# Kernel tuning notes

Hardware: AMD Instinct MI355X
Metric: run time of the kernel (lower is better)

## Reference

```python
import jax, jax.numpy as jnp
import numpy as np
from functools import partial

INPUT_DIM = 22
HIDDEN = 64
LAYERS = 3
OUT = 4
B, T = 1024, 512


def _lstm_layer(x_seq, w_ih, w_hh, b_ih, b_hh):
    # x_seq: [B, T, Din]; gate order (PyTorch): i, f, g, o
    Bsz = x_seq.shape[0]
    H = w_hh.shape[1]
    # precompute input projections for all timesteps: [B, T, 4H]
    x_proj = jnp.einsum('bti,gi->btg', x_seq, w_ih) + b_ih + b_hh

    def step(carry, xp):
        h, c = carry
        gates = xp + h @ w_hh.T  # [B, 4H]
        i, f, g, o = jnp.split(gates, 4, axis=-1)
        i = jax.nn.sigmoid(i)
        f = jax.nn.sigmoid(f)
        g = jnp.tanh(g)
        o = jax.nn.sigmoid(o)
        c = f * c + i * g
        h = o * jnp.tanh(c)
        return (h, c), h

    init = (jnp.zeros((Bsz, H), x_seq.dtype), jnp.zeros((Bsz, H), x_seq.dtype))
    _, hs = jax.lax.scan(step, init, jnp.swapaxes(x_proj, 0, 1))  # [T, B, H]
    return jnp.swapaxes(hs, 0, 1)  # [B, T, H]


def setup_inputs() -> dict:
    key = jax.random.key(0)
    ks = jax.random.split(key, 16)
    inp = {'x': jax.random.normal(ks[0], (B, INPUT_DIM, T), dtype=jnp.float32)}
    k = 1.0 / np.sqrt(HIDDEN)
    i = 1
    for l in range(LAYERS):
        din = INPUT_DIM if l == 0 else HIDDEN
        inp[f'w_ih{l}'] = jax.random.uniform(ks[i], (4 * HIDDEN, din), minval=-k, maxval=k); i += 1
        inp[f'w_hh{l}'] = jax.random.uniform(ks[i], (4 * HIDDEN, HIDDEN), minval=-k, maxval=k); i += 1
        inp[f'b_ih{l}'] = jax.random.uniform(ks[i], (4 * HIDDEN,), minval=-k, maxval=k); i += 1
        inp[f'b_hh{l}'] = jax.random.uniform(ks[i], (4 * HIDDEN,), minval=-k, maxval=k); i += 1
    inp['w_fc'] = jax.random.uniform(ks[i], (OUT, HIDDEN), minval=-k, maxval=k); i += 1
    inp['b_fc'] = jax.random.uniform(ks[i], (OUT,), minval=-k, maxval=k)
    return inp


def reference(x, w_ih0, w_hh0, b_ih0, b_hh0, w_ih1, w_hh1, b_ih1, b_hh1,
              w_ih2, w_hh2, b_ih2, b_hh2, w_fc, b_fc):
    # x: [B, 22, T] -> batch_first [B, T, 22]
    h = jnp.transpose(x, (0, 2, 1))
    h = _lstm_layer(h, w_ih0, w_hh0, b_ih0, b_hh0)
    # inter-layer dropout(0.4) is identity in eval/inference mode
    h = _lstm_layer(h, w_ih1, w_hh1, b_ih1, b_hh1)
    h = _lstm_layer(h, w_ih2, w_hh2, b_ih2, b_hh2)
    last = h[:, -1, :]  # [B, H]
    return last @ w_fc.T + b_fc  # [B, 4]
```

## Files before the change

### kernel.cpp

```cpp
#include <hip/hip_runtime.h>


#define TT   512
#define NTH  768
#define NBLK 256

typedef _Float16 h16;
typedef __attribute__((ext_vector_type(8))) _Float16 h16x8;
typedef __attribute__((ext_vector_type(4))) float f32x4;

#define MFMA16(a, b, c) __builtin_amdgcn_mfma_f32_16x16x32_f16((a), (b), (c), 0, 0, 0)

__device__ __forceinline__ float sigm(float z) {
    return __builtin_amdgcn_rcpf(1.f + __expf(-z));
}

__device__ __forceinline__ h16x8 loadB(const float* __restrict__ W, int ld, int ro,
                                       int k0, int kmax) {
    h16x8 r;
    #pragma unroll
    for (int i = 0; i < 8; ++i) {
        const int k = k0 + i;
        r[i] = (h16)((k < kmax) ? W[(size_t)ro * ld + k] : 0.f);
    }
    return r;
}

__global__ __attribute__((amdgpu_flat_work_group_size(NTH, NTH), amdgpu_waves_per_eu(3)))
void lstm_mfma(
    const float* __restrict__ x,
    const float* __restrict__ wih0, const float* __restrict__ whh0,
    const float* __restrict__ bih0, const float* __restrict__ bhh0,
    const float* __restrict__ wih1, const float* __restrict__ whh1,
    const float* __restrict__ bih1, const float* __restrict__ bhh1,
    const float* __restrict__ wih2, const float* __restrict__ whh2,
    const float* __restrict__ bih2, const float* __restrict__ bhh2,
    const float* __restrict__ wfc, const float* __restrict__ bfc,
    float* __restrict__ out)
{
    const int tid  = threadIdx.x;
    const int w    = tid >> 6;
    const int wl   = w >> 2;
    const int wg   = w & 3;
    const int lane = tid & 63;
    const int nloc = lane & 15;
    const int kg   = lane >> 4;
    const int b4   = blockIdx.x * 4;
    const int u    = wg * 16 + nloc;

    __shared__ alignas(16) h16 XL[2 * 32 * 512];
    __shared__ alignas(16) h16 HT[3 * 2 * 1024];
    __shared__ h16 PAD[3072];

    h16x8 Bf[4][4];
    float bias[4];
    #pragma unroll
    for (int g = 0; g < 4; ++g) {
        const int ro = g * 64 + u;
        if (wl == 0) {
            Bf[g][0] = loadB(wih0, 22, ro, kg * 8,      22);
            Bf[g][1] = loadB(whh0, 64, ro, kg * 8,      64);
            Bf[g][2] = loadB(whh0, 64, ro, 32 + kg * 8, 64);
            Bf[g][3] = Bf[g][2];
            bias[g]  = bih0[ro] + bhh0[ro];
        } else if (wl == 1) {
            Bf[g][0] = loadB(wih1, 64, ro, kg * 8,      64);
            Bf[g][1] = loadB(wih1, 64, ro, 32 + kg * 8, 64);
            Bf[g][2] = loadB(whh1, 64, ro, kg * 8,      64);
            Bf[g][3] = loadB(whh1, 64, ro, 32 + kg * 8, 64);
            bias[g]  = bih1[ro] + bhh1[ro];
        } else {
            Bf[g][0] = loadB(wih2, 64, ro, kg * 8,      64);
            Bf[g][1] = loadB(wih2, 64, ro, 32 + kg * 8, 64);
            Bf[g][2] = loadB(whh2, 64, ro, kg * 8,      64);
            Bf[g][3] = loadB(whh2, 64, ro, 32 + kg * 8, 64);
            bias[g]  = bih2[ro] + bhh2[ro];
        }
    }

    if (bias[0] > 1.0e30f) { PAD[tid & 2047] = (h16)bias[0]; out[0] = (float)PAD[0]; }

    {
        int* xz = (int*)XL;
        for (int i = tid; i < 2 * 32 * 256; i += NTH) xz[i] = 0;
        int* hz = (int*)HT;
        for (int i = tid; i < 3 * 2 * 512; i += NTH) hz[i] = 0;
    }
    __syncthreads();

    auto stage_x = [&](int chunk) {
        if (tid < 4 * 22) {
            const int bl = tid / 22, ii = tid - bl * 22;
            const float* src = x + (size_t)(b4 + bl) * (22 * 512) + (size_t)ii * 512
                                 + chunk * 32;
            h16* dst = &XL[(chunk & 1) * (32 * 512) + (ii >> 3) * 128 + (4 * bl) * 8 + (ii & 7)];
            #pragma unroll
            for (int q = 0; q < 8; ++q) {
                const float4 v = ((const float4*)src)[q];
                dst[(q * 4 + 0) * 512] = (h16)v.x;
                dst[(q * 4 + 1) * 512] = (h16)v.y;
                dst[(q * 4 + 2) * 512] = (h16)v.z;
                dst[(q * 4 + 3) * 512] = (h16)v.w;
            }
        }
    };
    stage_x(0);

    const int lo8  = lane * 8;
    const int hoff = (u >> 3) * 128 + kg * 32 + (u & 7);

    float cst = 0.f;

    auto ew = [&](const f32x4& zi, const f32x4& zf, const f32x4& zg, const f32x4& zo,
                  h16* hb) {
        const float vi = sigm(zi[0]);
        const float vf = sigm(zf[0]);
        const float vg = 2.f * sigm(2.f * zg[0]) - 1.f;
        const float vo = sigm(zo[0]);
        const float c  = vf * cst + vi * vg;
        cst = c;
        hb[hoff] = (h16)(vo * (2.f * sigm(2.f * c) - 1.f));
    };

    __syncthreads();

    #pragma unroll 1
    for (int t = 0; t < TT + 2; ++t) {
        const int wb = t & 1, rb = wb ^ 1;
        const h16* h0r = HT + 0 * 2048 + rb * 1024;
        h16*       h0w = HT + 0 * 2048 + wb * 1024;
        const h16* h1r = HT + 1 * 2048 + rb * 1024;
        h16*       h1w = HT + 1 * 2048 + wb * 1024;
        const h16* h2r = HT + 2 * 2048 + rb * 1024;
        h16*       h2w = HT + 2 * 2048 + wb * 1024;

        if (wl == 0) {
            if (t < TT) {
                const h16x8 ax   = *(const h16x8*)&XL[((t >> 5) & 1) * (32 * 512)
                                                      + (t & 31) * 512 + lo8];
                const h16x8 a0lo = *(const h16x8*)(h0r + lo8);
                const h16x8 a0hi = *(const h16x8*)(h0r + lo8 + 512);
                f32x4 z[4];
                #pragma unroll
                for (int g = 0; g < 4; ++g) {
                    z[g] = f32x4{bias[g], 0.f, 0.f, 0.f};
                    z[g] = MFMA16(ax,   Bf[g][0], z[g]);
                    z[g] = MFMA16(a0lo, Bf[g][1], z[g]);
                    z[g] = MFMA16(a0hi, Bf[g][2], z[g]);
                }
                ew(z[0], z[1], z[2], z[3], h0w);
            }
            if ((t & 31) == 16 && (t >> 5) < 15) stage_x((t >> 5) + 1);
        } else if (wl == 1) {
            if (t >= 1 && t < TT + 1) {
                const h16x8 a0lo = *(const h16x8*)(h0r + lo8);
                const h16x8 a0hi = *(const h16x8*)(h0r + lo8 + 512);
                const h16x8 a1lo = *(const h16x8*)(h1r + lo8);
                const h16x8 a1hi = *(const h16x8*)(h1r + lo8 + 512);
                f32x4 z[4];
                #pragma unroll
                for (int g = 0; g < 4; ++g) {
                    z[g] = f32x4{bias[g], 0.f, 0.f, 0.f};
                    z[g] = MFMA16(a0lo, Bf[g][0], z[g]);
                    z[g] = MFMA16(a0hi, Bf[g][1], z[g]);
                    z[g] = MFMA16(a1lo, Bf[g][2], z[g]);
                    z[g] = MFMA16(a1hi, Bf[g][3], z[g]);
                }
                ew(z[0], z[1], z[2], z[3], h1w);
            }
        } else {
            if (t >= 2) {
                const h16x8 a1lo = *(const h16x8*)(h1r + lo8);
                const h16x8 a1hi = *(const h16x8*)(h1r + lo8 + 512);
                const h16x8 a2lo = *(const h16x8*)(h2r + lo8);
                const h16x8 a2hi = *(const h16x8*)(h2r + lo8 + 512);
                f32x4 z[4];
                #pragma unroll
                for (int g = 0; g < 4; ++g) {
                    z[g] = f32x4{bias[g], 0.f, 0.f, 0.f};
                    z[g] = MFMA16(a1lo, Bf[g][0], z[g]);
                    z[g] = MFMA16(a1hi, Bf[g][1], z[g]);
                    z[g] = MFMA16(a2lo, Bf[g][2], z[g]);
                    z[g] = MFMA16(a2hi, Bf[g][3], z[g]);
                }
                ew(z[0], z[1], z[2], z[3], h2w);
            }
        }

        __syncthreads();
    }

    if (tid < 16) {
        const int ms = tid >> 2, o = tid & 3;
        const h16* h2 = HT + 2 * 2048 + 1024;
        float acc = bfc[o];
        #pragma unroll 1
        for (int uu = 0; uu < 64; ++uu)
            acc += (float)h2[(uu >> 3) * 128 + (4 * ms) * 8 + (uu & 7)] * wfc[o * 64 + uu];
        out[(b4 + ms) * 4 + o] = acc;
    }
}

extern "C" void kernel_launch(void* const* d_in, const int* in_sizes, int n_in,
                              void* d_out, int out_size, void* d_ws, size_t ws_size,
                              hipStream_t stream) {
    const float* x    = (const float*)d_in[0];
    const float* wih0 = (const float*)d_in[1];
    const float* whh0 = (const float*)d_in[2];
    const float* bih0 = (const float*)d_in[3];
    const float* bhh0 = (const float*)d_in[4];
    const float* wih1 = (const float*)d_in[5];
    const float* whh1 = (const float*)d_in[6];
    const float* bih1 = (const float*)d_in[7];
    const float* bhh1 = (const float*)d_in[8];
    const float* wih2 = (const float*)d_in[9];
    const float* whh2 = (const float*)d_in[10];
    const float* bih2 = (const float*)d_in[11];
    const float* bhh2 = (const float*)d_in[12];
    const float* wfc  = (const float*)d_in[13];
    const float* bfc  = (const float*)d_in[14];
    float* out = (float*)d_out;

    lstm_mfma<<<dim3(NBLK), dim3(NTH), 0, stream>>>(
        x, wih0, whh0, bih0, bhh0, wih1, whh1, bih1, bhh1,
        wih2, whh2, bih2, bhh2, wfc, bfc, out);
}
```

Before: 421.5 us.

## Precompute next-step input projections off the recurrent critical path with deeper skew

Each layer's wavefronts now compute the input-projection MFMAs for the next timestep (into a carried accumulator) while only the two recurrent MFMAs per gate sit on the dependency chain before the elementwise update. The hidden-state buffers become 4-deep rings and the layer skew widens to two steps so the cross-layer input is available one step early. The goal is a shorter per-timestep serial chain ahead of the barrier, at the cost of more LDS and registers, a few extra loop iterations, and removal of the LDS padding trick that limited occupancy.

After: 476.9 us. 1.13x slower.

```diff
diff --git a/kernel.cpp b/kernel.cpp
--- a/kernel.cpp
+++ b/kernel.cpp
@@ -49,42 +49,43 @@
     const int u    = wg * 16 + nloc;
 
     __shared__ alignas(16) h16 XL[2 * 32 * 512];
-    __shared__ alignas(16) h16 HT[3 * 2 * 1024];
-    __shared__ h16 PAD[3072];
-
-    h16x8 Bf[4][4];
+    __shared__ alignas(16) h16 HT[3 * 4 * 1024];
+
+    h16x8 Bc[4][2], Bs[4][2];
     float bias[4];
     #pragma unroll
     for (int g = 0; g < 4; ++g) {
         const int ro = g * 64 + u;
         if (wl == 0) {
-            Bf[g][0] = loadB(wih0, 22, ro, kg * 8,      22);
-            Bf[g][1] = loadB(whh0, 64, ro, kg * 8,      64);
-            Bf[g][2] = loadB(whh0, 64, ro, 32 + kg * 8, 64);
-            Bf[g][3] = Bf[g][2];
+            Bc[g][0] = loadB(wih0, 22, ro, kg * 8,      22);
+            Bc[g][1] = Bc[g][0];
+            Bs[g][0] = loadB(whh0, 64, ro, kg * 8,      64);
+            Bs[g][1] = loadB(whh0, 64, ro, 32 + kg * 8, 64);
             bias[g]  = bih0[ro] + bhh0[ro];
         } else if (wl == 1) {
-            Bf[g][0] = loadB(wih1, 64, ro, kg * 8,      64);
-            Bf[g][1] = loadB(wih1, 64, ro, 32 + kg * 8, 64);
-            Bf[g][2] = loadB(whh1, 64, ro, kg * 8,      64);
-            Bf[g][3] = loadB(whh1, 64, ro, 32 + kg * 8, 64);
+            Bc[g][0] = loadB(wih1, 64, ro, kg * 8,      64);
+            Bc[g][1] = loadB(wih1, 64, ro, 32 + kg * 8, 64);
+            Bs[g][0] = loadB(whh1, 64, ro, kg * 8,      64);
+            Bs[g][1] = loadB(whh1, 64, ro, 32 + kg * 8, 64);
             bias[g]  = bih1[ro] + bhh1[ro];
         } else {
-            Bf[g][0] = loadB(wih2, 64, ro, kg * 8,      64);
-            Bf[g][1] = loadB(wih2, 64, ro, 32 + kg * 8, 64);
-            Bf[g][2] = loadB(whh2, 64, ro, kg * 8,      64);
-            Bf[g][3] = loadB(whh2, 64, ro, 32 + kg * 8, 64);
+            Bc[g][0] = loadB(wih2, 64, ro, kg * 8,      64);
+            Bc[g][1] = loadB(wih2, 64, ro, 32 + kg * 8, 64);
+            Bs[g][0] = loadB(whh2, 64, ro, kg * 8,      64);
+            Bs[g][1] = loadB(whh2, 64, ro, 32 + kg * 8, 64);
             bias[g]  = bih2[ro] + bhh2[ro];
         }
     }
 
-    if (bias[0] > 1.0e30f) { PAD[tid & 2047] = (h16)bias[0]; out[0] = (float)PAD[0]; }
+    f32x4 bz[4];
+    #pragma unroll
+    for (int g = 0; g < 4; ++g) { bz[g][0] = bias[g]; bz[g][1] = 0.f; bz[g][2] = 0.f; bz[g][3] = 0.f; }
 
     {
         int* xz = (int*)XL;
         for (int i = tid; i < 2 * 32 * 256; i += NTH) xz[i] = 0;
         int* hz = (int*)HT;
-        for (int i = tid; i < 3 * 2 * 512; i += NTH) hz[i] = 0;
+        for (int i = tid; i < 3 * 4 * 512; i += NTH) hz[i] = 0;
     }
     __syncthreads();
 
@@ -108,8 +109,14 @@
 
     const int lo8  = lane * 8;
     const int hoff = (u >> 3) * 128 + kg * 32 + (u & 7);
+    h16* const HT0 = HT;
+    h16* const HT1 = HT + 4096;
+    h16* const HT2 = HT + 8192;
 
     float cst = 0.f;
+    f32x4 zc[4];
+    #pragma unroll
+    for (int g = 0; g < 4; ++g) zc[g] = bz[g];
 
     auto ew = [&](const f32x4& zi, const f32x4& zf, const f32x4& zg, const f32x4& zo,
                   h16* hb) {
@@ -124,67 +131,84 @@
 
     __syncthreads();
 
+    if (wl == 0) {
+        const h16x8 ax = *(const h16x8*)&XL[lo8];
+        #pragma unroll
+        for (int g = 0; g < 4; ++g) zc[g] = MFMA16(ax, Bc[g][0], zc[g]);
+    }
+
     #pragma unroll 1
-    for (int t = 0; t < TT + 2; ++t) {
-        const int wb = t & 1, rb = wb ^ 1;
-        const h16* h0r = HT + 0 * 2048 + rb * 1024;
-        h16*       h0w = HT + 0 * 2048 + wb * 1024;
-        const h16* h1r = HT + 1 * 2048 + rb * 1024;
-        h16*       h1w = HT + 1 * 2048 + wb * 1024;
-        const h16* h2r = HT + 2 * 2048 + rb * 1024;
-        h16*       h2w = HT + 2 * 2048 + wb * 1024;
-
+    for (int t = 0; t < TT + 4; ++t) {
         if (wl == 0) {
             if (t < TT) {
-                const h16x8 ax   = *(const h16x8*)&XL[((t >> 5) & 1) * (32 * 512)
-                                                      + (t & 31) * 512 + lo8];
-                const h16x8 a0lo = *(const h16x8*)(h0r + lo8);
-                const h16x8 a0hi = *(const h16x8*)(h0r + lo8 + 512);
+                const h16* hs = HT0 + ((t - 1) & 3) * 1024;
+                const h16x8 aSlo = *(const h16x8*)(hs + lo8);
+                const h16x8 aShi = *(const h16x8*)(hs + lo8 + 512);
                 f32x4 z[4];
                 #pragma unroll
                 for (int g = 0; g < 4; ++g) {
-                    z[g] = f32x4{bias[g], 0.f, 0.f, 0.f};
-                    z[g] = MFMA16(ax,   Bf[g][0], z[g]);
-                    z[g] = MFMA16(a0lo, Bf[g][1], z[g]);
-                    z[g] = MFMA16(a0hi, Bf[g][2], z[g]);
-                }
-                ew(z[0], z[1], z[2], z[3], h0w);
+                    z[g] = MFMA16(aSlo, Bs[g][0], zc[g]);
+                    z[g] = MFMA16(aShi, Bs[g][1], z[g]);
+                }
+                if (t + 1 < TT) {
+                    const int tp = t + 1;
+                    const h16x8 ax = *(const h16x8*)&XL[((tp >> 5) & 1) * (32 * 512)
+                                                        + (tp & 31) * 512 + lo8];
+                    #pragma unroll
+                    for (int g = 0; g < 4; ++g)
+                        zc[g] = MFMA16(ax, Bc[g][0], bz[g]);
+                }
+                ew(z[0], z[1], z[2], z[3], HT0 + (t & 3) * 1024);
             }
             if ((t & 31) == 16 && (t >> 5) < 15) stage_x((t >> 5) + 1);
         } else if (wl == 1) {
+            const bool doew = (t >= 2 && t < TT + 2);
+            f32x4 z[4];
+            if (doew) {
+                const h16* hs = HT1 + ((t - 3) & 3) * 1024;
+                const h16x8 aSlo = *(const h16x8*)(hs + lo8);
+                const h16x8 aShi = *(const h16x8*)(hs + lo8 + 512);
+                #pragma unroll
+                for (int g = 0; g < 4; ++g) {
+                    z[g] = MFMA16(aSlo, Bs[g][0], zc[g]);
+                    z[g] = MFMA16(aShi, Bs[g][1], z[g]);
+                }
+            }
             if (t >= 1 && t < TT + 1) {
-                const h16x8 a0lo = *(const h16x8*)(h0r + lo8);
-                const h16x8 a0hi = *(const h16x8*)(h0r + lo8 + 512);
-                const h16x8 a1lo = *(const h16x8*)(h1r + lo8);
-                const h16x8 a1hi = *(const h16x8*)(h1r + lo8 + 512);
-                f32x4 z[4];
-                #pragma unroll
-                for (int g = 0; g < 4; ++g) {
-                    z[g] = f32x4{bias[g], 0.f, 0.f, 0.f};
-                    z[g] = MFMA16(a0lo, Bf[g][0], z[g]);
-                    z[g] = MFMA16(a0hi, Bf[g][1], z[g]);
-                    z[g] = MFMA16(a1lo, Bf[g][2], z[g]);
-                    z[g] = MFMA16(a1hi, Bf[g][3], z[g]);
-                }
-                ew(z[0], z[1], z[2], z[3], h1w);
-            }
+                const h16* hc = HT0 + ((t - 1) & 3) * 1024;
+                const h16x8 aClo = *(const h16x8*)(hc + lo8);
+                const h16x8 aChi = *(const h16x8*)(hc + lo8 + 512);
+                #pragma unroll
+                for (int g = 0; g < 4; ++g) {
+                    zc[g] = MFMA16(aClo, Bc[g][0], bz[g]);
+                    zc[g] = MFMA16(aChi, Bc[g][1], zc[g]);
+                }
+            }
+            if (doew) ew(z[0], z[1], z[2], z[3], HT1 + ((t - 2) & 3) * 1024);
         } else {
-            if (t >= 2) {
-                const h16x8 a1lo = *(const h16x8*)(h1r + lo8);
-                const h16x8 a1hi = *(const h16x8*)(h1r + lo8 + 512);
-                const h16x8 a2lo = *(const h16x8*)(h2r + lo8);
-                const h16x8 a2hi = *(const h16x8*)(h2r + lo8 + 512);
-                f32x4 z[4];
-                #pragma unroll
-                for (int g = 0; g < 4; ++g) {
-                    z[g] = f32x4{bias[g], 0.f, 0.f, 0.f};
-                    z[g] = MFMA16(a1lo, Bf[g][0], z[g]);
-                    z[g] = MFMA16(a1hi, Bf[g][1], z[g]);
-                    z[g] = MFMA16(a2lo, Bf[g][2], z[g]);
-                    z[g] = MFMA16(a2hi, Bf[g][3], z[g]);
-                }
-                ew(z[0], z[1], z[2], z[3], h2w);
-            }
+            const bool doew = (t >= 4);
+            f32x4 z[4];
+            if (doew) {
+                const h16* hs = HT2 + ((t - 5) & 3) * 1024;
+                const h16x8 aSlo = *(const h16x8*)(hs + lo8);
+                const h16x8 aShi = *(const h16x8*)(hs + lo8 + 512);
+                #pragma unroll
+                for (int g = 0; g < 4; ++g) {
+                    z[g] = MFMA16(aSlo, Bs[g][0], zc[g]);
+                    z[g] = MFMA16(aShi, Bs[g][1], z[g]);
+                }
+            }
+            if (t >= 3 && t < TT + 3) {
+                const h16* hc = HT1 + ((t - 3) & 3) * 1024;
+                const h16x8 aClo = *(const h16x8*)(hc + lo8);
+                const h16x8 aChi = *(const h16x8*)(hc + lo8 + 512);
+                #pragma unroll
+                for (int g = 0; g < 4; ++g) {
+                    zc[g] = MFMA16(aClo, Bc[g][0], bz[g]);
+                    zc[g] = MFMA16(aChi, Bc[g][1], zc[g]);
+                }
+            }
+            if (doew) ew(z[0], z[1], z[2], z[3], HT2 + ((t - 4) & 3) * 1024);
         }
 
         __syncthreads();
@@ -192,7 +216,7 @@
 
     if (tid < 16) {
         const int ms = tid >> 2, o = tid & 3;
-        const h16* h2 = HT + 2 * 2048 + 1024;
+        const h16* h2 = HT2 + 3 * 1024;
         float acc = bfc[o];
         #pragma unroll 1
         for (int uu = 0; uu < 64; ++uu)
```

## Replace per-step block barriers with LDS progress-counter flags between layer wave groups

Applied to the files above, without the earlier changes.

Drops the __syncthreads at every timestep. Each layer's four waves now publish a per-wave progress counter in shared memory and spin on the counters of the groups they depend on. The hidden-state buffers become 4-deep rings, so layers can drift up to three steps apart and pipeline more loosely. The risks are spin-wait overhead and LDS polling contention, plus the memory-ordering subtlety of using volatile flags with block-level fences. It also drops the dummy PAD shared allocation and hoists the bias vectors out of the loop.

New measurement: 511.1 us. 1.21x slower.

```diff
diff --git a/kernel.cpp b/kernel.cpp
--- a/kernel.cpp
+++ b/kernel.cpp
@@ -49,8 +49,8 @@
     const int u    = wg * 16 + nloc;
 
     __shared__ alignas(16) h16 XL[2 * 32 * 512];
-    __shared__ alignas(16) h16 HT[3 * 2 * 1024];
-    __shared__ h16 PAD[3072];
+    __shared__ alignas(16) h16 HT[3 * 4 * 1024];
+    __shared__ unsigned PROG[12];
 
     h16x8 Bf[4][4];
     float bias[4];
@@ -77,14 +77,16 @@
             bias[g]  = bih2[ro] + bhh2[ro];
         }
     }
-
-    if (bias[0] > 1.0e30f) { PAD[tid & 2047] = (h16)bias[0]; out[0] = (float)PAD[0]; }
+    f32x4 bz[4];
+    #pragma unroll
+    for (int g = 0; g < 4; ++g) { bz[g][0] = bias[g]; bz[g][1] = 0.f; bz[g][2] = 0.f; bz[g][3] = 0.f; }
 
     {
         int* xz = (int*)XL;
         for (int i = tid; i < 2 * 32 * 256; i += NTH) xz[i] = 0;
         int* hz = (int*)HT;
-        for (int i = tid; i < 3 * 2 * 512; i += NTH) hz[i] = 0;
+        for (int i = tid; i < 3 * 4 * 512; i += NTH) hz[i] = 0;
+        if (tid < 12) PROG[tid] = 0;
     }
     __syncthreads();
 
@@ -105,9 +107,13 @@
         }
     };
     stage_x(0);
+    __syncthreads();
 
     const int lo8  = lane * 8;
     const int hoff = (u >> 3) * 128 + kg * 32 + (u & 7);
+    h16* const HT0 = HT;
+    h16* const HT1 = HT + 4096;
+    h16* const HT2 = HT + 8192;
 
     float cst = 0.f;
 
@@ -122,77 +128,107 @@
         hb[hoff] = (h16)(vo * (2.f * sigm(2.f * c) - 1.f));
     };
 
-    __syncthreads();
-
-    #pragma unroll 1
-    for (int t = 0; t < TT + 2; ++t) {
-        const int wb = t & 1, rb = wb ^ 1;
-        const h16* h0r = HT + 0 * 2048 + rb * 1024;
-        h16*       h0w = HT + 0 * 2048 + wb * 1024;
-        const h16* h1r = HT + 1 * 2048 + rb * 1024;
-        h16*       h1w = HT + 1 * 2048 + wb * 1024;
-        const h16* h2r = HT + 2 * 2048 + rb * 1024;
-        h16*       h2w = HT + 2 * 2048 + wb * 1024;
-
-        if (wl == 0) {
-            if (t < TT) {
-                const h16x8 ax   = *(const h16x8*)&XL[((t >> 5) & 1) * (32 * 512)
-                                                      + (t & 31) * 512 + lo8];
-                const h16x8 a0lo = *(const h16x8*)(h0r + lo8);
-                const h16x8 a0hi = *(const h16x8*)(h0r + lo8 + 512);
-                f32x4 z[4];
-                #pragma unroll
-                for (int g = 0; g < 4; ++g) {
-                    z[g] = f32x4{bias[g], 0.f, 0.f, 0.f};
-                    z[g] = MFMA16(ax,   Bf[g][0], z[g]);
-                    z[g] = MFMA16(a0lo, Bf[g][1], z[g]);
-                    z[g] = MFMA16(a0hi, Bf[g][2], z[g]);
-                }
-                ew(z[0], z[1], z[2], z[3], h0w);
-            }
+    auto waitge = [&](int grp, int need) {
+        if (need <= 0) return;
+        volatile unsigned* p = (volatile unsigned*)&PROG[4 * grp];
+        for (;;) {
+            unsigned a = p[0], b = p[1], c = p[2], d = p[3];
+            unsigned m = a < b ? a : b;
+            unsigned n = c < d ? c : d;
+            m = m < n ? m : n;
+            if ((int)m >= need) return;
+            __builtin_amdgcn_s_sleep(1);
+        }
+    };
+    auto publish = [&](int val) {
+        __threadfence_block();
+        if (lane == 0) ((volatile unsigned*)PROG)[w] = (unsigned)val;
+    };
+
+    if (wl == 0) {
+        #pragma unroll 1
+        for (int t = 0; t < TT; ++t) {
+            waitge(0, t);
+            waitge(1, t - 3);
+            __threadfence_block();
+            const h16* hs = HT0 + ((t - 1) & 3) * 1024;
+            const h16x8 ax   = *(const h16x8*)&XL[((t >> 5) & 1) * (32 * 512)
+                                                  + (t & 31) * 512 + lo8];
+            const h16x8 aSlo = *(const h16x8*)(hs + lo8);
+            const h16x8 aShi = *(const h16x8*)(hs + lo8 + 512);
+            f32x4 z[4];
+            #pragma unroll
+            for (int g = 0; g < 4; ++g) {
+                z[g] = MFMA16(ax,   Bf[g][0], bz[g]);
+                z[g] = MFMA16(aSlo, Bf[g][1], z[g]);
+                z[g] = MFMA16(aShi, Bf[g][2], z[g]);
+            }
+            ew(z[0], z[1], z[2], z[3], HT0 + (t & 3) * 1024);
+            publish(t + 1);
             if ((t & 31) == 16 && (t >> 5) < 15) stage_x((t >> 5) + 1);
-        } else if (wl == 1) {
-            if (t >= 1 && t < TT + 1) {
-                const h16x8 a0lo = *(const h16x8*)(h0r + lo8);
-                const h16x8 a0hi = *(const h16x8*)(h0r + lo8 + 512);
-                const h16x8 a1lo = *(const h16x8*)(h1r + lo8);
-                const h16x8 a1hi = *(const h16x8*)(h1r + lo8 + 512);
-                f32x4 z[4];
-                #pragma unroll
-                for (int g = 0; g < 4; ++g) {
-                    z[g] = f32x4{bias[g], 0.f, 0.f, 0.f};
-                    z[g] = MFMA16(a0lo, Bf[g][0], z[g]);
-                    z[g] = MFMA16(a0hi, Bf[g][1], z[g]);
-                    z[g] = MFMA16(a1lo, Bf[g][2], z[g]);
-                    z[g] = MFMA16(a1hi, Bf[g][3], z[g]);
-                }
-                ew(z[0], z[1], z[2], z[3], h1w);
-            }
-        } else {
-            if (t >= 2) {
-                const h16x8 a1lo = *(const h16x8*)(h1r + lo8);
-                const h16x8 a1hi = *(const h16x8*)(h1r + lo8 + 512);
-                const h16x8 a2lo = *(const h16x8*)(h2r + lo8);
-                const h16x8 a2hi = *(const h16x8*)(h2r + lo8 + 512);
-                f32x4 z[4];
-                #pragma unroll
-                for (int g = 0; g < 4; ++g) {
-                    z[g] = f32x4{bias[g], 0.f, 0.f, 0.f};
-                    z[g] = MFMA16(a1lo, Bf[g][0], z[g]);
-                    z[g] = MFMA16(a1hi, Bf[g][1], z[g]);
-                    z[g] = MFMA16(a2lo, Bf[g][2], z[g]);
-                    z[g] = MFMA16(a2hi, Bf[g][3], z[g]);
-                }
-                ew(z[0], z[1], z[2], z[3], h2w);
-            }
-        }
-
-        __syncthreads();
+        }
+    } else if (wl == 1) {
+        #pragma unroll 1
+        for (int t = 0; t < TT; ++t) {
+            waitge(0, t + 1);
+            waitge(1, t);
+            waitge(2, t - 3);
+            __threadfence_block();
+            const h16* hc = HT0 + (t & 3) * 1024;
+            const h16* hs = HT1 + ((t - 1) & 3) * 1024;
+            const h16x8 aClo = *(const h16x8*)(hc + lo8);
+            const h16x8 aChi = *(const h16x8*)(hc + lo8 + 512);
+            const h16x8 aSlo = *(const h16x8*)(hs + lo8);
+            const h16x8 aShi = *(const h16x8*)(hs + lo8 + 512);
+            f32x4 z[4];
+            #pragma unroll
+            for (int g = 0; g < 4; ++g) {
+                z[g] = MFMA16(aClo, Bf[g][0], bz[g]);
+                z[g] = MFMA16(aChi, Bf[g][1], z[g]);
+                z[g] = MFMA16(aSlo, Bf[g][2], z[g]);
+                z[g] = MFMA16(aShi, Bf[g][3], z[g]);
+            }
+            ew(z[0], z[1], z[2], z[3], HT1 + (t & 3) * 1024);
+            publish(t + 1);
+        }
+    } else {
+        #pragma unroll 1
+        for (int t = 0; t < TT; ++t) {
+            waitge(1, t + 1);
+            waitge(2, t);
+            __threadfence_block();
+            const h16* hc = HT1 + (t & 3) * 1024;
+            const h16* hs = HT2 + ((t - 1) & 3) * 1024;
+            const h16x8 aClo = *(const h16x8*)(hc + lo8);
+            const h16x8 aChi = *(const h16x8*)(hc + lo8 + 512);
+            const h16x8 aSlo = *(const h16x8*)(hs + lo8);
+            const h16x8 aShi = *(const h16x8*)(hs + lo8 + 512);
+            f32x4 z[4];
+            #pragma unroll
+            for (int g = 0; g < 4; ++g) {
+                z[g] = MFMA16(aClo, Bf[g][0], bz[g]);
+                z[g] = MFMA16(aChi, Bf[g][1], z[g]);
+                z[g] = MFMA16(aSlo, Bf[g][2], z[g]);
+                z[g] = MFMA16(aShi, Bf[g][3], z[g]);
+            }
+            ew(z[0], z[1], z[2], z[3], HT2 + (t & 3) * 1024);
+            publish(t + 1);
+        }
     }
 
     if (tid < 16) {
+        volatile unsigned* p = (volatile unsigned*)&PROG[8];
+        for (;;) {
+            unsigned a = p[0], b = p[1], c = p[2], d = p[3];
+            unsigned m = a < b ? a : b;
+            unsigned n = c < d ? c : d;
+            m = m < n ? m : n;
+            if (m >= (unsigned)TT) break;
+            __builtin_amdgcn_s_sleep(1);
+        }
+        __threadfence_block();
         const int ms = tid >> 2, o = tid & 3;
-        const h16* h2 = HT + 2 * 2048 + 1024;
+        const h16* h2 = HT2 + ((TT - 1) & 3) * 1024;
         float acc = bfc[o];
         #pragma unroll 1
         for (int uu = 0; uu < 64; ++uu)
```
